# Kernel tuning notes

Hardware: AMD Instinct MI355X
Metric: run time of the kernel (lower is better)

The kernel has to match this reference:

```python
import jax, jax.numpy as jnp
import numpy as np

HIDDEN = 1024
HEADS = 8
HEAD = HIDDEN // HEADS
EPS = 1e-5


def _gammas():
    lo = np.log(1.0 / 512.0)
    hi = np.log(1.0 / 32.0)
    lin = np.linspace(lo, hi, HEADS)
    return jnp.asarray(1.0 - np.exp(lin), dtype=jnp.float32)  # [H]


def setup_inputs() -> dict:
    key = jax.random.key(0)
    ks = jax.random.split(key, 7)
    B, S = 2, 2048
    x = jax.random.normal(ks[0], (B, S, HIDDEN), dtype=jnp.float32)
    # Per-head retention projection weights (Retention(head_size, gamma)): [H, d, d]
    Wq = jax.random.normal(ks[1], (HEADS, HEAD, HEAD), dtype=jnp.float32) / HEAD
    Wk = jax.random.normal(ks[2], (HEADS, HEAD, HEAD), dtype=jnp.float32) / HEAD
    Wv = jax.random.normal(ks[3], (HEADS, HEAD, HEAD), dtype=jnp.float32) / HEAD
    W1 = jax.random.normal(ks[4], (HIDDEN, HIDDEN), dtype=jnp.float32) / HIDDEN
    W2 = jax.random.normal(ks[5], (HIDDEN, HIDDEN), dtype=jnp.float32) / HIDDEN
    gn_w = jnp.ones((HIDDEN,), dtype=jnp.float32)
    gn_b = jnp.zeros((HIDDEN,), dtype=jnp.float32)
    return {"x": x, "Wq": Wq, "Wk": Wk, "Wv": Wv, "W1": W1, "W2": W2,
            "gn_w": gn_w, "gn_b": gn_b}


def _decay_mask(S, gammas):
    idx = jnp.arange(S)
    diff = idx[:, None] - idx[None, :]              # [S, S]
    causal = diff >= 0
    safe = jnp.where(causal, diff, 0).astype(jnp.float32)
    D = jnp.where(causal[None], gammas[:, None, None] ** safe[None], 0.0)  # [H,S,S]
    return D


def _msr_forward(x, Wq, Wk, Wv, W1, W2, gn_w, gn_b):
    B, S, _ = x.shape
    xh = x.reshape(B, S, HEADS, HEAD)               # per-head slices
    q = jnp.einsum('bshd,hde->bshe', xh, Wq)
    k = jnp.einsum('bshd,hde->bshe', xh, Wk)
    v = jnp.einsum('bshd,hde->bshe', xh, Wv)
    D = _decay_mask(S, _gammas())                   # [H,S,S]
    scores = jnp.einsum('bnhd,bmhd->bhnm', q, k) * D[None]
    ret = jnp.einsum('bhnm,bmhd->bnhd', scores, v)  # [B,S,H,d]
    # GroupNorm(num_groups=H, channels=HIDDEN) over flattened rows
    mu = jnp.mean(ret, axis=-1, keepdims=True)
    var = jnp.var(ret, axis=-1, keepdims=True)
    ret = (ret - mu) * jax.lax.rsqrt(var + EPS)
    ret = ret.reshape(B, S, HIDDEN) * gn_w + gn_b
    gated = x @ W1
    out = gated * jax.nn.sigmoid(gated) + ret       # swish gate + residual add
    return out @ W2


def reference(x, Wq, Wk, Wv, W1, W2, gn_w, gn_b):
    return _msr_forward(x, Wq, Wk, Wv, W1, W2, gn_w, gn_b)
```

## Files before the change

### kernel.cpp

```cpp
#include <hip/hip_runtime.h>
#include <hip/hip_bf16.h>

#define HID 1024
#define NH 8
#define HD 128
#define BB 2
#define SS 2048
#define CHK 128
#define NCH 16

typedef __attribute__((ext_vector_type(8))) short short8;
typedef __attribute__((ext_vector_type(4))) float f32x4;

static __device__ __forceinline__ float b2f(unsigned short u){
  unsigned int x = ((unsigned int)u) << 16; float f;
  __builtin_memcpy(&f, &x, 4); return f;
}
static __device__ __forceinline__ unsigned short f2b(float f){
  unsigned int x; __builtin_memcpy(&x, &f, 4);
  x += 0x7fffu + ((x >> 16) & 1u);
  return (unsigned short)(x >> 16);
}
static __device__ __forceinline__ float head_gamma(int h){
  double lo = -6.238324625039508;
  double hi = -3.4657359027997265;
  double lin = lo + (hi - lo) * ((double)h / 7.0);
  return (float)(1.0 - exp(lin));
}
static __device__ __forceinline__ f32x4 MFMA(short8 a, short8 b, f32x4 c){
  return __builtin_amdgcn_mfma_f32_16x16x32_bf16(a, b, c, 0, 0, 0);
}

typedef const __attribute__((address_space(1))) unsigned int* gas1_u32p;
typedef __attribute__((address_space(3))) unsigned int* las3_u32p;
static __device__ __forceinline__ void gload_lds16(const void* g, void* l){
  __builtin_amdgcn_global_load_lds((gas1_u32p)g, (las3_u32p)l, 16, 0, 0);
}

__global__ __launch_bounds__(256) void k_prep(
    const float* __restrict__ x,  unsigned short* __restrict__ xb,
    const float* __restrict__ W1, unsigned short* __restrict__ w1T,
    const float* __restrict__ W2, unsigned short* __restrict__ w2T,
    const float* __restrict__ Wq, unsigned short* __restrict__ wqT,
    const float* __restrict__ Wk, unsigned short* __restrict__ wkT,
    const float* __restrict__ Wv, unsigned short* __restrict__ wvT)
{
  int bid = blockIdx.x, t = threadIdx.x;
  if (bid < 1024){
    const int n = BB*SS*HID;
    int i = (bid*256 + t)*4;
    const int st = 1024*256*4;
    for (; i < n; i += st){
      float4 v = *(const float4*)(x + i);
      unsigned short o[4] = { f2b(v.x), f2b(v.y), f2b(v.z), f2b(v.w) };
      *(uint2*)(xb + i) = *(const uint2*)o;
    }
    return;
  }
  __shared__ float tile[32][33];
  const float* in; unsigned short* out; int R, C, r0, c0;
  if (bid < 3072){
    int which = (bid - 1024) >> 10;
    int local = (bid - 1024) & 1023;
    in  = which ? W2 : W1;  out = which ? w2T : w1T;
    R = C = HID;
    c0 = (local & 31)*32; r0 = (local >> 5)*32;
  } else {
    int local = bid - 3072;
    int mat = local >> 7;
    int rem = local & 127;
    int z = rem >> 4, tl2 = rem & 15;
    const float* ws[3] = { Wq, Wk, Wv };
    unsigned short* os[3] = { wqT, wkT, wvT };
    in  = ws[mat] + (size_t)z*HD*HD;
    out = os[mat] + (size_t)z*HD*HD;
    R = C = HD;
    c0 = (tl2 & 3)*32; r0 = (tl2 >> 2)*32;
  }
  int tx = t & 31, ty = t >> 5;
  #pragma unroll
  for (int i=0;i<4;i++) tile[ty+i*8][tx] = in[(size_t)(r0+ty+i*8)*C + c0+tx];
  __syncthreads();
  #pragma unroll
  for (int i=0;i<4;i++) out[(size_t)(c0+ty+i*8)*R + r0+tx] = f2b(tile[tx][ty+i*8]);
}

__global__ __launch_bounds__(256) void k_qkv(
    const unsigned short* __restrict__ xb,
    const unsigned short* __restrict__ wqT,
    const unsigned short* __restrict__ wkT,
    const unsigned short* __restrict__ wvT,
    unsigned short* __restrict__ qb,
    unsigned short* __restrict__ kb,
    unsigned short* __restrict__ ktsb,
    unsigned short* __restrict__ vtb)
{
  int bid = blockIdx.x;
  int stile = bid & 31;
  int bh = bid >> 5;
  int h = bh & 7, b = bh >> 3;
  int T0 = stile*64;
  int chunk = stile >> 1, pm0 = (stile & 1)*64;
  float l2g = log2f(head_gamma(h));
  __shared__ unsigned short tl[128*72];
  int t = threadIdx.x, wv = t>>6, l = t&63, lr = l&15, lg = l>>4;
  int row0 = T0 + wv*16;
  short8 a[4];
  const unsigned short* xp = xb + (size_t)(b*SS + row0 + lr)*HID + h*HD + lg*8;
  #pragma unroll
  for (int kk=0;kk<4;kk++) a[kk] = *(const short8*)(xp + kk*32);
  size_t obase = ((size_t)bh*SS + row0)*HD;
  size_t tbase = ((size_t)(bh*NCH + chunk))*HD*CHK + pm0;

  auto wout = [&](unsigned short* dst){
    int e = t & 127, th = t >> 7;
    const uint4* src = (const uint4*)(tl + e*72 + th*32);
    uint4* d4 = (uint4*)(dst + (size_t)e*CHK + th*32);
    #pragma unroll
    for (int i=0;i<4;i++) d4[i] = src[i];
  };

  {
    const unsigned short* wb = wqT + (size_t)h*HD*HD;
    unsigned short* op = qb + obase;
    #pragma unroll
    for (int nt=0;nt<8;nt++){
      f32x4 acc = {0.f,0.f,0.f,0.f};
      #pragma unroll
      for (int kk=0;kk<4;kk++){
        short8 bfr = *(const short8*)(wb + (size_t)(nt*16+lr)*HD + kk*32 + lg*8);
        acc = MFMA(a[kk], bfr, acc);
      }
      #pragma unroll
      for (int r=0;r<4;r++)
        op[(size_t)(lg*4+r)*HD + nt*16 + lr] = f2b(acc[r]);
    }
  }
  {
    const unsigned short* wb = wkT + (size_t)h*HD*HD;
    unsigned short* op = kb + obase;
    float ksc[4];
    #pragma unroll
    for (int r=0;r<4;r++)
      ksc[r] = exp2f((float)(127 - (pm0 + wv*16 + lg*4 + r))*l2g);
    #pragma unroll
    for (int nt=0;nt<8;nt++){
      f32x4 acc = {0.f,0.f,0.f,0.f};
      #pragma unroll
      for (int kk=0;kk<4;kk++){
        short8 bfr = *(const short8*)(wb + (size_t)(nt*16+lr)*HD + kk*32 + lg*8);
        acc = MFMA(a[kk], bfr, acc);
      }
      #pragma unroll
      for (int r=0;r<4;r++){
        op[(size_t)(lg*4+r)*HD + nt*16 + lr] = f2b(acc[r]);
        tl[(nt*16+lr)*72 + wv*16 + lg*4 + r] = f2b(acc[r]*ksc[r]);
      }
    }
  }
  __syncthreads();
  wout(ktsb + tbase);
  __syncthreads();
  {
    const unsigned short* wb = wvT + (size_t)h*HD*HD;
    #pragma unroll
    for (int nt=0;nt<8;nt++){
      f32x4 acc = {0.f,0.f,0.f,0.f};
      #pragma unroll
      for (int kk=0;kk<4;kk++){
        short8 bfr = *(const short8*)(wb + (size_t)(nt*16+lr)*HD + kk*32 + lg*8);
        acc = MFMA(a[kk], bfr, acc);
      }
      #pragma unroll
      for (int r=0;r<4;r++)
        tl[(nt*16+lr)*72 + wv*16 + lg*4 + r] = f2b(acc[r]);
    }
  }
  __syncthreads();
  wout(vtb + tbase);
}

__global__ __launch_bounds__(256) void k_sumscan(
    const unsigned short* __restrict__ ktsb,
    const unsigned short* __restrict__ vtb,
    unsigned short* __restrict__ ST)
{
  int bid = blockIdx.x;
  int dh = bid & 1, et = (bid >> 1) & 7, bh = bid >> 4;
  int h = bh & 7;
  float d128 = exp2f(128.f * log2f(head_gamma(h)));
  int t = threadIdx.x, wv = t>>6, l = t&63, lr = l&15, lg = l>>4;
  int e0 = et*16;
  int d0w = dh*64 + wv*16;
  const unsigned short* vt = vtb  + (size_t)bh*NCH*HD*CHK;
  const unsigned short* kt = ktsb + (size_t)bh*NCH*HD*CHK;
  unsigned short* Sb = ST + (size_t)bh*NCH*HD*HD;

  f32x4 s = {0.f,0.f,0.f,0.f};
  #pragma unroll
  for (int c=0;c<NCH;c++){
    const unsigned short* vc = vt + (size_t)c*HD*CHK;
    const unsigned short* kc = kt + (size_t)c*HD*CHK;
    f32x4 acc = {0.f,0.f,0.f,0.f};
    #pragma unroll
    for (int kk=0;kk<4;kk++){
      short8 af = *(const short8*)(vc + (size_t)(e0+lr)*CHK + kk*32 + lg*8);
      short8 bf = *(const short8*)(kc + (size_t)(d0w+lr)*CHK + kk*32 + lg*8);
      acc = MFMA(af, bf, acc);
    }
    unsigned short* So = Sb + (size_t)c*HD*HD;
    #pragma unroll
    for (int r=0;r<4;r++){
      So[(size_t)(e0+lg*4+r)*HD + d0w + lr] = f2b(s[r]);
      s[r] = s[r]*d128 + acc[r];
    }
  }
}

__global__ __launch_bounds__(512) void k_g1ret(
    const unsigned short* __restrict__ A,
    const unsigned short* __restrict__ BT,
    const unsigned short* __restrict__ qb,
    const unsigned short* __restrict__ kb,
    const unsigned short* __restrict__ vtb,
    const unsigned short* __restrict__ ST,
    const float* __restrict__ gnw,
    const float* __restrict__ gnb,
    unsigned short* __restrict__ Cb,
    int M, int N, int K)
{
  __shared__ unsigned short ls[4][2][128*64];
  const int nb = N >> 7;
  const int nwg = (M >> 7) * nb;
  const int cpx = nwg >> 3;
  int bid0 = blockIdx.x;
  int bid = (bid0 & 7)*cpx + (bid0 >> 3);
  const int m0 = (bid / nb) << 7;
  const int n0 = (bid % nb) << 7;
  const int t = threadIdx.x, wv = t>>6, l = t&63, lr = l&15, lg = l>>4;
  const int wr = (wv>>1)<<5;
  const int wc = (wv&1)<<6;
  const int srow = l >> 3;
  const int sgc  = ((l & 7) ^ srow) << 3;
  const unsigned short* Abase = A  + (size_t)(m0 + wv*16 + srow)*K + sgc;
  const unsigned short* Bbase = BT + (size_t)(n0 + wv*16 + srow)*K + sgc;

  auto stage = [&](int buf, int kt){
    unsigned short* la = &ls[buf][0][0];
    unsigned short* lb = &ls[buf][1][0];
    int k0 = kt << 6;
    #pragma unroll
    for (int it=0; it<2; ++it){
      gload_lds16(Abase + (size_t)(it*8)*K + k0, la + (wv*16 + it*8)*64);
      gload_lds16(Bbase + (size_t)(it*8)*K + k0, lb + (wv*16 + it*8)*64);
    }
  };

  const int b = m0 >> 11, j = (m0 >> 7) & 15, h = n0 >> 7;
  const int bh = b*NH + h;
  const int cj = bh*NCH + j;
  float l2g = log2f(head_gamma(h));
  const unsigned short* qc = qb + ((size_t)bh*SS + j*CHK)*HD;
  const unsigned short* kc = kb + ((size_t)bh*SS + j*CHK)*HD;
  const unsigned short* vt = vtb + (size_t)cj*HD*CHK;
  const unsigned short* Sp = ST + (size_t)cj*HD*HD;

  short8 qf[4];
  #pragma unroll
  for (int kk=0;kk<4;kk++)
    qf[kk] = *(const short8*)(qc + (size_t)(wv*16 + lr)*HD + kk*32 + lg*8);

  stage(0,0); stage(1,1); stage(2,2);

  f32x4 racc[8];
  #pragma unroll
  for (int nt=0;nt<8;nt++){
    f32x4 aa = {0,0,0,0};
    #pragma unroll
    for (int kk=0;kk<4;kk++){
      short8 bfr = *(const short8*)(Sp + (size_t)(nt*16+lr)*HD + kk*32 + lg*8);
      aa = MFMA(qf[kk], bfr, aa);
    }
    racc[nt] = aa;
  }
  #pragma unroll
  for (int r=0;r<4;r++){
    int n = wv*16 + lg*4 + r;
    float sf = exp2f((float)(n+1)*l2g);
    #pragma unroll
    for (int nt=0;nt<8;nt++) racc[nt][r] *= sf;
  }

  f32x4 acc[2][4];
  #pragma unroll
  for (int i=0;i<2;i++)
    #pragma unroll
    for (int j2=0;j2<4;j2++) acc[i][j2] = (f32x4){0,0,0,0};

  const int NT = K >> 6;
  for (int kt = 0; kt < NT; ++kt){
    if (kt < NT-2)       asm volatile("s_waitcnt vmcnt(8)" ::: "memory");
    else if (kt == NT-2) asm volatile("s_waitcnt vmcnt(4)" ::: "memory");
    else                 asm volatile("s_waitcnt vmcnt(0)" ::: "memory");
    __builtin_amdgcn_s_barrier();
    __builtin_amdgcn_sched_barrier(0);
    if (kt+3 < NT) stage((kt+3)&3, kt+3);
    const unsigned short* pa = &ls[kt&3][0][0];
    const unsigned short* pb = &ls[kt&3][1][0];
    #pragma unroll
    for (int ks=0; ks<2; ++ks){
      short8 af[2], bf[4];
      #pragma unroll
      for (int i=0;i<2;i++){
        int ra = wr + i*16 + lr;
        af[i] = *(const short8*)(pa + ra*64 + ((((ks<<2)+lg) ^ (ra&7))<<3));
      }
      #pragma unroll
      for (int j2=0;j2<4;j2++){
        int rb = wc + j2*16 + lr;
        bf[j2] = *(const short8*)(pb + rb*64 + ((((ks<<2)+lg) ^ (rb&7))<<3));
      }
      #pragma unroll
      for (int i=0;i<2;i++)
        #pragma unroll
        for (int j2=0;j2<4;j2++)
          acc[i][j2] = MFMA(af[i], bf[j2], acc[i][j2]);
    }
  }
  __syncthreads();

  unsigned short* ct = (unsigned short*)&ls[0][0][0];
  unsigned short* sc = ct + 128*136;
  #pragma unroll
  for (int i=0;i<2;i++){
    #pragma unroll
    for (int j2=0;j2<4;j2++){
      #pragma unroll
      for (int r=0;r<4;r++){
        int row = wr + i*16 + lg*4 + r;
        int col = wc + j2*16 + lr;
        float v = acc[i][j2][r];
        ct[row*136 + col] = f2b(v / (1.f + __expf(-v)));
      }
    }
  }
  __syncthreads();

  int ntmax = (wv | 1) + 1;
  for (int nt=0; nt<ntmax; nt++){
    f32x4 a0 = {0,0,0,0};
    #pragma unroll
    for (int kk=0;kk<4;kk++){
      short8 bfr = *(const short8*)(kc + (size_t)(nt*16+lr)*HD + kk*32 + lg*8);
      a0 = MFMA(qf[kk], bfr, a0);
    }
    int col = nt*16 + lr;
    #pragma unroll
    for (int r=0;r<4;r++){
      int n = wv*16 + lg*4 + r;
      float v0 = (col <= n) ? a0[r]*exp2f((float)(n-col)*l2g) : 0.f;
      sc[(wv*16 + lg*4 + r)*136 + col] = f2b(v0);
    }
  }

  int ksmax = (wv >> 1) + 1;
  for (int ks=0; ks<ksmax; ks++){
    short8 afr = *(const short8*)&sc[(wv*16 + lr)*136 + ks*32 + lg*8];
    #pragma unroll
    for (int nt=0;nt<8;nt++){
      short8 bfr = *(const short8*)(vt + (size_t)(nt*16+lr)*CHK + ks*32 + lg*8);
      racc[nt] = MFMA(afr, bfr, racc[nt]);
    }
  }

  unsigned short* op = Cb + (size_t)(m0 + wv*16)*N + n0;
  const float* gw  = gnw + h*HD;
  const float* gbb = gnb + h*HD;
  #pragma unroll
  for (int r=0;r<4;r++){
    float s = 0.f, ss = 0.f;
    #pragma unroll
    for (int nt=0;nt<8;nt++){ float x = racc[nt][r]; s += x; ss += x*x; }
    #pragma unroll
    for (int off=1; off<16; off<<=1){
      s  += __shfl_xor(s,  off, 64);
      ss += __shfl_xor(ss, off, 64);
    }
    float mu  = s*(1.f/128.f);
    float var = ss*(1.f/128.f) - mu*mu;
    float rs  = rsqrtf(var + 1e-5f);
    int lrow = lg*4 + r;
    unsigned short* orow = op + (size_t)lrow*N;
    #pragma unroll
    for (int nt=0;nt<8;nt++){
      int col = nt*16 + lr;
      float rv = (racc[nt][r]-mu)*rs*gw[col] + gbb[col];
      orow[col] = f2b(rv + b2f(ct[(wv*16 + lrow)*136 + col]));
    }
  }
}

__global__ __launch_bounds__(512) void k_gemm2(
    const unsigned short* __restrict__ A,
    const unsigned short* __restrict__ BT,
    float* __restrict__ Cf,
    int M, int N, int K)
{
  __shared__ unsigned short ls[4][2][128*64];
  const int nb = N >> 7;
  const int nwg = (M >> 7) * nb;
  const int cpx = nwg >> 3;
  int bid0 = blockIdx.x;
  int bid = (bid0 & 7)*cpx + (bid0 >> 3);
  const int m0 = (bid / nb) << 7;
  const int n0 = (bid % nb) << 7;
  const int t = threadIdx.x, wv = t>>6, l = t&63, lr = l&15, lg = l>>4;
  const int wr = (wv>>1)<<5;
  const int wc = (wv&1)<<6;
  const int srow = l >> 3;
  const int sgc  = ((l & 7) ^ srow) << 3;
  const unsigned short* Abase = A  + (size_t)(m0 + wv*16 + srow)*K + sgc;
  const unsigned short* Bbase = BT + (size_t)(n0 + wv*16 + srow)*K + sgc;

  auto stage = [&](int buf, int kt){
    unsigned short* la = &ls[buf][0][0];
    unsigned short* lb = &ls[buf][1][0];
    int k0 = kt << 6;
    #pragma unroll
    for (int it=0; it<2; ++it){
      gload_lds16(Abase + (size_t)(it*8)*K + k0, la + (wv*16 + it*8)*64);
      gload_lds16(Bbase + (size_t)(it*8)*K + k0, lb + (wv*16 + it*8)*64);
    }
  };

  f32x4 acc[2][4];
  #pragma unroll
  for (int i=0;i<2;i++)
    #pragma unroll
    for (int j=0;j<4;j++) acc[i][j] = (f32x4){0,0,0,0};

  const int NT = K >> 6;
  stage(0,0); stage(1,1); stage(2,2);
  for (int kt = 0; kt < NT; ++kt){
    if (kt < NT-2)       asm volatile("s_waitcnt vmcnt(8)" ::: "memory");
    else if (kt == NT-2) asm volatile("s_waitcnt vmcnt(4)" ::: "memory");
    else                 asm volatile("s_waitcnt vmcnt(0)" ::: "memory");
    __builtin_amdgcn_s_barrier();
    __builtin_amdgcn_sched_barrier(0);
    if (kt+3 < NT) stage((kt+3)&3, kt+3);
    const unsigned short* pa = &ls[kt&3][0][0];
    const unsigned short* pb = &ls[kt&3][1][0];
    #pragma unroll
    for (int ks=0; ks<2; ++ks){
      short8 af[2], bf[4];
      #pragma unroll
      for (int i=0;i<2;i++){
        int ra = wr + i*16 + lr;
        af[i] = *(const short8*)(pa + ra*64 + ((((ks<<2)+lg) ^ (ra&7))<<3));
      }
      #pragma unroll
      for (int j=0;j<4;j++){
        int rb = wc + j*16 + lr;
        bf[j] = *(const short8*)(pb + rb*64 + ((((ks<<2)+lg) ^ (rb&7))<<3));
      }
      #pragma unroll
      for (int i=0;i<2;i++)
        #pragma unroll
        for (int j=0;j<4;j++)
          acc[i][j] = MFMA(af[i], bf[j], acc[i][j]);
    }
  }

  #pragma unroll
  for (int i=0;i<2;i++)
    #pragma unroll
    for (int j=0;j<4;j++)
      #pragma unroll
      for (int r=0;r<4;r++){
        int row = m0 + wr + i*16 + lg*4 + r;
        int col = n0 + wc + j*16 + lr;
        Cf[(size_t)row*N + col] = acc[i][j][r];
      }
}

extern "C" void kernel_launch(void* const* d_in, const int* in_sizes, int n_in,
                              void* d_out, int out_size, void* d_ws, size_t ws_size,
                              hipStream_t stream)
{
  (void)in_sizes; (void)n_in; (void)out_size; (void)ws_size;
  const float* x   = (const float*)d_in[0];
  const float* Wq  = (const float*)d_in[1];
  const float* Wk  = (const float*)d_in[2];
  const float* Wv  = (const float*)d_in[3];
  const float* W1  = (const float*)d_in[4];
  const float* W2  = (const float*)d_in[5];
  const float* gnw = (const float*)d_in[6];
  const float* gnb = (const float*)d_in[7];
  float* out = (float*)d_out;

  char* wsp = (char*)d_ws;
  size_t off = 0;
  auto alloc = [&](size_t bytes)->void*{
    off = (off + 255) & ~(size_t)255;
    void* p = wsp + off; off += bytes; return p;
  };
  const size_t NTOK = (size_t)BB*SS;
  unsigned short* xb   = (unsigned short*)alloc(NTOK*HID*2);
  unsigned short* w1T  = (unsigned short*)alloc((size_t)HID*HID*2);
  unsigned short* w2T  = (unsigned short*)alloc((size_t)HID*HID*2);
  unsigned short* wqT  = (unsigned short*)alloc((size_t)NH*HD*HD*2);
  unsigned short* wkT  = (unsigned short*)alloc((size_t)NH*HD*HD*2);
  unsigned short* wvT  = (unsigned short*)alloc((size_t)NH*HD*HD*2);
  unsigned short* qb   = (unsigned short*)alloc(NTOK*HID*2);
  unsigned short* kb   = (unsigned short*)alloc(NTOK*HID*2);
  unsigned short* ktsb = (unsigned short*)alloc(NTOK*HID*2);
  unsigned short* vtb  = (unsigned short*)alloc(NTOK*HID*2);
  unsigned short* ST   = (unsigned short*)alloc((size_t)BB*NH*NCH*HD*HD*2);
  unsigned short* opb  = (unsigned short*)alloc(NTOK*HID*2);

  k_prep<<<dim3(3456), dim3(256), 0, stream>>>(x, xb, W1, w1T, W2, w2T,
                                               Wq, wqT, Wk, wkT, Wv, wvT);
  k_qkv<<<dim3(BB*NH*32), dim3(256), 0, stream>>>(xb, wqT, wkT, wvT, qb, kb, ktsb, vtb);
  k_sumscan<<<dim3(BB*NH*16), dim3(256), 0, stream>>>(ktsb, vtb, ST);

  k_g1ret<<<dim3(256), dim3(512), 0, stream>>>(xb, w1T, qb, kb, vtb, ST, gnw, gnb,
                                               opb, (int)NTOK, HID, HID);
  k_gemm2<<<dim3(256), dim3(512), 0, stream>>>(opb, w2T, out, (int)NTOK, HID, HID);
}
```

Before: 111.3 us.

## Prefetch state, V and K chunk tiles into LDS during final GEMM iterations

The fused gate-GEMM plus retention kernel now issues async global-to-LDS loads of the state matrix, transposed V and K chunk tiles during the last three K-loop iterations, using an XOR-swizzled layout. The intra-chunk and cross-chunk retention MFMAs then read their B operands from LDS instead of scattered global loads. The state-times-Q product moves after the GEMM loop, which frees its accumulator registers during the main loop. The cost is extra barriers and a more intricate LDS reuse plan across the four 16K-element regions.

```diff
diff --git a/kernel.cpp b/kernel.cpp
--- a/kernel.cpp
+++ b/kernel.cpp
@@ -229,7 +229,7 @@
     unsigned short* __restrict__ Cb,
     int M, int N, int K)
 {
-  __shared__ unsigned short ls[4][2][128*64];
+  __shared__ unsigned short lsu[65536];
   const int nb = N >> 7;
   const int nwg = (M >> 7) * nb;
   const int cpx = nwg >> 3;
@@ -246,13 +246,22 @@
   const unsigned short* Bbase = BT + (size_t)(n0 + wv*16 + srow)*K + sgc;
 
   auto stage = [&](int buf, int kt){
-    unsigned short* la = &ls[buf][0][0];
-    unsigned short* lb = &ls[buf][1][0];
+    unsigned short* la = lsu + buf*16384;
+    unsigned short* lb = la + 8192;
     int k0 = kt << 6;
     #pragma unroll
     for (int it=0; it<2; ++it){
       gload_lds16(Abase + (size_t)(it*8)*K + k0, la + (wv*16 + it*8)*64);
       gload_lds16(Bbase + (size_t)(it*8)*K + k0, lb + (wv*16 + it*8)*64);
+    }
+  };
+  auto stageMat = [&](const unsigned short* g, int reg){
+    #pragma unroll
+    for (int i=0;i<4;i++){
+      int c = i*512 + t;
+      int row = c >> 4, p = c & 15;
+      gload_lds16(g + row*128 + ((p ^ (row & 7)) << 3),
+                  lsu + reg + (i*512 + (t & 448))*8);
     }
   };
 
@@ -270,34 +279,14 @@
   for (int kk=0;kk<4;kk++)
     qf[kk] = *(const short8*)(qc + (size_t)(wv*16 + lr)*HD + kk*32 + lg*8);
 
+  f32x4 acc[2][4];
+  #pragma unroll
+  for (int i=0;i<2;i++)
+    #pragma unroll
+    for (int j2=0;j2<4;j2++) acc[i][j2] = (f32x4){0,0,0,0};
+
+  const int NT = K >> 6;
   stage(0,0); stage(1,1); stage(2,2);
-
-  f32x4 racc[8];
-  #pragma unroll
-  for (int nt=0;nt<8;nt++){
-    f32x4 aa = {0,0,0,0};
-    #pragma unroll
-    for (int kk=0;kk<4;kk++){
-      short8 bfr = *(const short8*)(Sp + (size_t)(nt*16+lr)*HD + kk*32 + lg*8);
-      aa = MFMA(qf[kk], bfr, aa);
-    }
-    racc[nt] = aa;
-  }
-  #pragma unroll
-  for (int r=0;r<4;r++){
-    int n = wv*16 + lg*4 + r;
-    float sf = exp2f((float)(n+1)*l2g);
-    #pragma unroll
-    for (int nt=0;nt<8;nt++) racc[nt][r] *= sf;
-  }
-
-  f32x4 acc[2][4];
-  #pragma unroll
-  for (int i=0;i<2;i++)
-    #pragma unroll
-    for (int j2=0;j2<4;j2++) acc[i][j2] = (f32x4){0,0,0,0};
-
-  const int NT = K >> 6;
   for (int kt = 0; kt < NT; ++kt){
     if (kt < NT-2)       asm volatile("s_waitcnt vmcnt(8)" ::: "memory");
     else if (kt == NT-2) asm volatile("s_waitcnt vmcnt(4)" ::: "memory");
@@ -305,8 +294,11 @@
     __builtin_amdgcn_s_barrier();
     __builtin_amdgcn_sched_barrier(0);
     if (kt+3 < NT) stage((kt+3)&3, kt+3);
-    const unsigned short* pa = &ls[kt&3][0][0];
-    const unsigned short* pb = &ls[kt&3][1][0];
+    if (kt == NT-3) stageMat(Sp, 0);
+    if (kt == NT-2) stageMat(vt, 16384);
+    if (kt == NT-1) stageMat(kc, 32768);
+    const unsigned short* pa = lsu + (kt&3)*16384;
+    const unsigned short* pb = pa + 8192;
     #pragma unroll
     for (int ks=0; ks<2; ++ks){
       short8 af[2], bf[4];
@@ -329,8 +321,43 @@
   }
   __syncthreads();
 
-  unsigned short* ct = (unsigned short*)&ls[0][0][0];
-  unsigned short* sc = ct + 128*136;
+  f32x4 racc[8];
+  #pragma unroll
+  for (int nt=0;nt<8;nt++){
+    f32x4 aa = {0,0,0,0};
+    #pragma unroll
+    for (int kk=0;kk<4;kk++){
+      short8 bfr = *(const short8*)(lsu + (nt*16+lr)*128 + (((kk*4+lg) ^ (lr&7))<<3));
+      aa = MFMA(qf[kk], bfr, aa);
+    }
+    racc[nt] = aa;
+  }
+  #pragma unroll
+  for (int r=0;r<4;r++){
+    int n = wv*16 + lg*4 + r;
+    float sf = exp2f((float)(n+1)*l2g);
+    #pragma unroll
+    for (int nt=0;nt<8;nt++) racc[nt][r] *= sf;
+  }
+  __syncthreads();
+
+  int ntmax = (wv | 1) + 1;
+  for (int nt=0; nt<ntmax; nt++){
+    f32x4 a0 = {0,0,0,0};
+    #pragma unroll
+    for (int kk=0;kk<4;kk++){
+      short8 bfr = *(const short8*)(lsu + 32768 + (nt*16+lr)*128 + (((kk*4+lg) ^ (lr&7))<<3));
+      a0 = MFMA(qf[kk], bfr, a0);
+    }
+    int col = nt*16 + lr;
+    #pragma unroll
+    for (int r=0;r<4;r++){
+      int lrow = wv*16 + lg*4 + r;
+      float v0 = (col <= lrow) ? a0[r]*exp2f((float)(lrow-col)*l2g) : 0.f;
+      lsu[lrow*128 + (((col>>3) ^ (lrow&7))<<3) + (col&7)] = f2b(v0);
+    }
+  }
+
   #pragma unroll
   for (int i=0;i<2;i++){
     #pragma unroll
@@ -340,38 +367,22 @@
         int row = wr + i*16 + lg*4 + r;
         int col = wc + j2*16 + lr;
         float v = acc[i][j2][r];
-        ct[row*136 + col] = f2b(v / (1.f + __expf(-v)));
-      }
-    }
-  }
-  __syncthreads();
-
-  int ntmax = (wv | 1) + 1;
-  for (int nt=0; nt<ntmax; nt++){
-    f32x4 a0 = {0,0,0,0};
-    #pragma unroll
-    for (int kk=0;kk<4;kk++){
-      short8 bfr = *(const short8*)(kc + (size_t)(nt*16+lr)*HD + kk*32 + lg*8);
-      a0 = MFMA(qf[kk], bfr, a0);
-    }
-    int col = nt*16 + lr;
-    #pragma unroll
-    for (int r=0;r<4;r++){
-      int n = wv*16 + lg*4 + r;
-      float v0 = (col <= n) ? a0[r]*exp2f((float)(n-col)*l2g) : 0.f;
-      sc[(wv*16 + lg*4 + r)*136 + col] = f2b(v0);
+        lsu[49152 + row*128 + (((col>>3) ^ (row&7))<<3) + (col&7)]
+          = f2b(v / (1.f + __expf(-v)));
+      }
     }
   }
 
   int ksmax = (wv >> 1) + 1;
   for (int ks=0; ks<ksmax; ks++){
-    short8 afr = *(const short8*)&sc[(wv*16 + lr)*136 + ks*32 + lg*8];
+    short8 afr = *(const short8*)(lsu + (wv*16+lr)*128 + (((ks*4+lg) ^ (lr&7))<<3));
     #pragma unroll
     for (int nt=0;nt<8;nt++){
-      short8 bfr = *(const short8*)(vt + (size_t)(nt*16+lr)*CHK + ks*32 + lg*8);
+      short8 bfr = *(const short8*)(lsu + 16384 + (nt*16+lr)*128 + (((ks*4+lg) ^ (lr&7))<<3));
       racc[nt] = MFMA(afr, bfr, racc[nt]);
     }
   }
+  __syncthreads();
 
   unsigned short* op = Cb + (size_t)(m0 + wv*16)*N + n0;
   const float* gw  = gnw + h*HD;
@@ -390,12 +401,14 @@
     float var = ss*(1.f/128.f) - mu*mu;
     float rs  = rsqrtf(var + 1e-5f);
     int lrow = lg*4 + r;
+    int Rr = wv*16 + lrow;
     unsigned short* orow = op + (size_t)lrow*N;
     #pragma unroll
     for (int nt=0;nt<8;nt++){
       int col = nt*16 + lr;
       float rv = (racc[nt][r]-mu)*rs*gw[col] + gbb[col];
-      orow[col] = f2b(rv + b2f(ct[(wv*16 + lrow)*136 + col]));
+      float cv = b2f(lsu[49152 + Rr*128 + (((col>>3) ^ (Rr&7))<<3) + (col&7)]);
+      orow[col] = f2b(rv + cv);
     }
   }
 }
```

Result: faster. 100.2 us, median of 2 (-10.0%).
